# Performance work log

Hardware: AMD Instinct MI355X
Metric: run time of the kernel (lower is better)

## Reference

```python
import jax, jax.numpy as jnp
import numpy as np

SET_NUM, SET_SIZE, C, H, F, L_LAYERS, N_BLOCKS = 2048, 36, 192, 8, 384, 8, 4
N = SET_NUM * SET_SIZE


def _ln(x, g, b, eps=1e-5):
    m = x.mean(-1, keepdims=True)
    v = ((x - m) ** 2).mean(-1, keepdims=True)
    return (x - m) * jax.lax.rsqrt(v + eps) * g + b


def setup_inputs() -> dict:
    key = jax.random.key(0)
    ks = jax.random.split(key, 32)
    src = jax.random.normal(ks[0], (N, C), dtype=jnp.float32)
    pos_embed = jax.random.normal(ks[1], (2, N, C), dtype=jnp.float32)
    # each (shift, set) index tensor is a permutation of arange(N) -> every voxel appears exactly once
    perms = [jax.random.permutation(ks[2 + j], N).reshape(SET_NUM, SET_SIZE) for j in range(4)]
    set_voxel_inds = jnp.stack([jnp.stack(perms[0:2]), jnp.stack(perms[2:4])]).astype(jnp.int32)
    set_voxel_masks = jnp.zeros((2, 2, SET_NUM, SET_SIZE), dtype=bool)

    def p(k, shape, std=0.02):
        return (jax.random.normal(k, shape) * std).astype(jnp.float32)

    inp = dict(src=src, pos_embed=pos_embed, set_voxel_inds=set_voxel_inds,
               set_voxel_masks=set_voxel_masks,
               in_proj_w=p(ks[6], (L_LAYERS, 3 * C, C)), in_proj_b=p(ks[7], (L_LAYERS, 3 * C)),
               out_w=p(ks[8], (L_LAYERS, C, C)), out_b=p(ks[9], (L_LAYERS, C)),
               lin1_w=p(ks[10], (L_LAYERS, F, C)), lin1_b=p(ks[11], (L_LAYERS, F)),
               lin2_w=p(ks[12], (L_LAYERS, C, F)), lin2_b=p(ks[13], (L_LAYERS, C)),
               ln1_g=jnp.ones((L_LAYERS, C)), ln1_b=jnp.zeros((L_LAYERS, C)),
               ln2_g=jnp.ones((L_LAYERS, C)), ln2_b=jnp.zeros((L_LAYERS, C)),
               enc_g=jnp.ones((L_LAYERS, C)), enc_b=jnp.zeros((L_LAYERS, C)),
               blk_g=jnp.ones((N_BLOCKS, C)), blk_b=jnp.zeros((N_BLOCKS, C)))
    return inp


def reference(src, pos_embed, set_voxel_inds, set_voxel_masks,
              in_proj_w, in_proj_b, out_w, out_b, lin1_w, lin1_b, lin2_w, lin2_b,
              ln1_g, ln1_b, ln2_g, ln2_b, enc_g, enc_b, blk_g, blk_b):
    n_vox = src.shape[0]
    Dh = C // H
    scale = 1.0 / np.sqrt(Dh)

    def set_attn(x, pos, inds, mask, li):
        g = x[inds]                      # (S,K,C) gather voxels into sets
        qk_in = g + pos[inds]
        Wq, Wk, Wv = jnp.split(in_proj_w[li], 3, axis=0)
        bq, bk, bv = jnp.split(in_proj_b[li], 3)
        S, K = inds.shape
        q = (qk_in @ Wq.T + bq).reshape(S, K, H, Dh)
        k = (qk_in @ Wk.T + bk).reshape(S, K, H, Dh)
        v = (g @ Wv.T + bv).reshape(S, K, H, Dh)
        scores = jnp.einsum('skhd,slhd->shkl', q, k) * scale
        scores = jnp.where(mask[:, None, None, :], -1e9, scores)
        attn = jax.nn.softmax(scores, axis=-1)
        o = jnp.einsum('shkl,slhd->skhd', attn, v).reshape(S, K, C)
        o = o @ out_w[li].T + out_b[li]
        # torch.unique + flipped scatter == take the first occurrence of each voxel index
        flat = inds.reshape(-1)
        first = jnp.full((n_vox,), flat.size, dtype=flat.dtype).at[flat].min(
            jnp.arange(flat.size, dtype=flat.dtype))
        src2 = o.reshape(-1, C)[first]
        x = _ln(x + src2, ln1_g[li], ln1_b[li])
        ff = jax.nn.gelu(x @ lin1_w[li].T + lin1_b[li], approximate=False) @ lin2_w[li].T + lin2_b[li]
        x = _ln(x + ff, ln2_g[li], ln2_b[li])
        return x

    out = src
    for block_id in range(N_BLOCKS):
        residual = out
        shift = block_id % 2
        for i in range(2):
            li = block_id * 2 + i
            identity = out
            out = set_attn(out, pos_embed[i], set_voxel_inds[shift, i],
                           set_voxel_masks[shift, i], li)
            out = _ln(out + identity, enc_g[li], enc_b[li])
        out = _ln(out + residual, blk_g[block_id], blk_b[block_id])
    return out
```

## Files before the change

### kernel.cpp

```cpp
#include <hip/hip_runtime.h>
#include <hip/hip_bf16.h>
#include <hip/hip_fp16.h>

#define SETS 2048
#define SS   36
#define CDIM 192
#define HEADS 8
#define DH   24
#define FDIM 384
#define NVOX (SETS*SS)
#define NBLOCKS 4

typedef __hip_bfloat16 bf16;
typedef _Float16 f16;
typedef __attribute__((ext_vector_type(2))) _Float16 h2v;
typedef __attribute__((ext_vector_type(4))) short s4v;
typedef __attribute__((ext_vector_type(8))) short s8v;
typedef __attribute__((ext_vector_type(4))) float f4v;

__device__ __forceinline__ float to_f(float x) { return x; }
__device__ __forceinline__ float to_f(bf16 x)  { return __bfloat162float(x); }

__device__ __forceinline__ short f2bf(float x) {
  bf16 h = __float2bfloat16(x);
  return *reinterpret_cast<short*>(&h);
}
__device__ __forceinline__ unsigned pack2(float a, float b) {
  return ((unsigned)(unsigned short)f2bf(a)) | (((unsigned)(unsigned short)f2bf(b)) << 16);
}

__device__ __forceinline__ float dot2(unsigned a, unsigned b, float acc) {
#if __has_builtin(__builtin_amdgcn_fdot2)
  return __builtin_amdgcn_fdot2(__builtin_bit_cast(h2v, a), __builtin_bit_cast(h2v, b), acc, false);
#else
  h2v ha = __builtin_bit_cast(h2v, a), hb = __builtin_bit_cast(h2v, b);
  return acc + (float)ha[0] * (float)hb[0] + (float)ha[1] * (float)hb[1];
#endif
}
__device__ __forceinline__ unsigned pkh(float a, float b) {
#if __has_builtin(__builtin_amdgcn_cvt_pkrtz)
  return __builtin_bit_cast(unsigned, __builtin_amdgcn_cvt_pkrtz(a, b));
#else
  h2v h; h[0] = (f16)a; h[1] = (f16)b;
  return __builtin_bit_cast(unsigned, h);
#endif
}
__device__ __forceinline__ unsigned permw(unsigned a, unsigned b, unsigned sel) {
#if __has_builtin(__builtin_amdgcn_perm)
  return __builtin_amdgcn_perm(b, a, sel);
#else
  if (sel == 0x05040100u) return (a & 0xffffu) | (b << 16);
  return (a >> 16) | (b & 0xffff0000u);
#endif
}

__device__ __forceinline__ float allreduce64(float v) {
  #pragma unroll
  for (int off = 32; off > 0; off >>= 1) v += __shfl_xor(v, off);
  return v;
}

__device__ __forceinline__ void ln3(float v[3], const float* g, const float* b, int t) {
  float s = allreduce64(v[0] + v[1] + v[2]);
  float m = s * (1.0f / 192.0f);
  float d0 = v[0] - m, d1 = v[1] - m, d2 = v[2] - m;
  float q = allreduce64(d0 * d0 + d1 * d1 + d2 * d2);
  float rs = rsqrtf(q * (1.0f / 192.0f) + 1e-5f);
  v[0] = d0 * rs * g[t]       + b[t];
  v[1] = d1 * rs * g[t + 64]  + b[t + 64];
  v[2] = d2 * rs * g[t + 128] + b[t + 128];
}

__global__ __launch_bounds__(256) void wconv_k(const float* __restrict__ in,
                                               bf16* __restrict__ out, int n8) {
  int i = blockIdx.x * 256 + threadIdx.x;
  if (i < n8) {
    const float4* p = (const float4*)in + (size_t)i * 2;
    float4 a = p[0], b = p[1];
    s8v o;
    o[0] = f2bf(a.x); o[1] = f2bf(a.y); o[2] = f2bf(a.z); o[3] = f2bf(a.w);
    o[4] = f2bf(b.x); o[5] = f2bf(b.y); o[6] = f2bf(b.z); o[7] = f2bf(b.w);
    ((s8v*)out)[i] = o;
  }
}

__global__ __launch_bounds__(256) void init_k(const float* __restrict__ src,
    const float* __restrict__ pos0, float* __restrict__ a0,
    bf16* __restrict__ xb, bf16* __restrict__ xpb) {
  int i = blockIdx.x * 256 + threadIdx.x;
  float4 s = ((const float4*)src)[i];
  float4 p = ((const float4*)pos0)[i];
  ((float4*)a0)[i] = s;
  s4v ob, op;
  ob[0] = f2bf(s.x); ob[1] = f2bf(s.y); ob[2] = f2bf(s.z); ob[3] = f2bf(s.w);
  op[0] = f2bf(s.x + p.x); op[1] = f2bf(s.y + p.y);
  op[2] = f2bf(s.z + p.z); op[3] = f2bf(s.w + p.w);
  ((s4v*)xb)[i]  = ob;
  ((s4v*)xpb)[i] = op;
}

template<typename TO> __device__ __forceinline__ TO fcast(float v);
template<> __device__ __forceinline__ bf16 fcast<bf16>(float v) { return __float2bfloat16(v); }
template<> __device__ __forceinline__ f16  fcast<f16>(float v)  { return (f16)v; }

template<typename TO, int KT, int BM, int BN, int WM, int WN, bool GATHER, bool GELU_ACT>
__global__ __launch_bounds__(WM*WN*64) void bgemm_k(
    const bf16* __restrict__ A, const bf16* __restrict__ W,
    const float* __restrict__ bias, TO* __restrict__ Cmat,
    const int* __restrict__ idx, int ldc, int c_off)
{
  constexpr int NTHR = WM * WN * 64;
  constexpr int LD = 40;
  constexpr int MI = BM / (16 * WM);
  constexpr int NJ = BN / (16 * WN);
  constexpr int AC = BM * 4 / NTHR;
  constexpr int BC = BN * 4 / NTHR;
  constexpr int NT = KT / 32;
  static_assert(AC * NTHR == BM * 4 && BC * NTHR == BN * 4, "staging chunks");

  __shared__ short As[2][BM * LD];
  __shared__ short Bs[2][BN * LD];

  const int tid = threadIdx.x;
  const int n0 = blockIdx.x * BN;
  const int m0 = blockIdx.y * BM;
  const int wave = tid >> 6, lane = tid & 63;
  const int quad = lane >> 4, l16 = lane & 15;
  const int wm = (wave / WN) * (MI * 16);
  const int wn = (wave % WN) * (NJ * 16);

  const bf16* Aptr[AC]; int aoff[AC];
  #pragma unroll
  for (int c = 0; c < AC; c++) {
    int u = tid + c * NTHR;
    int row = u >> 2, c4 = u & 3;
    long arow = GATHER ? (long)idx[m0 + row] : (long)(m0 + row);
    Aptr[c] = A + arow * (long)KT + c4 * 8;
    aoff[c] = row * LD + c4 * 8;
  }
  const bf16* Bptr[BC]; int boff[BC];
  #pragma unroll
  for (int c = 0; c < BC; c++) {
    int u = tid + c * NTHR;
    int row = u >> 2, c4 = u & 3;
    Bptr[c] = W + (long)(n0 + row) * KT + c4 * 8;
    boff[c] = row * LD + c4 * 8;
  }

  uint4 ra[AC], rb[BC];
  #pragma unroll
  for (int c = 0; c < AC; c++) ra[c] = *(const uint4*)(Aptr[c]);
  #pragma unroll
  for (int c = 0; c < BC; c++) rb[c] = *(const uint4*)(Bptr[c]);
  #pragma unroll
  for (int c = 0; c < AC; c++) *(uint4*)&As[0][aoff[c]] = ra[c];
  #pragma unroll
  for (int c = 0; c < BC; c++) *(uint4*)&Bs[0][boff[c]] = rb[c];
  __syncthreads();

  f4v acc[MI][NJ];
  #pragma unroll
  for (int i = 0; i < MI; i++)
    #pragma unroll
    for (int j = 0; j < NJ; j++)
      #pragma unroll
      for (int r = 0; r < 4; r++) acc[i][j][r] = 0.f;

  #pragma unroll
  for (int t = 0; t < NT; t++) {
    const int cur = t & 1;
    if (t + 1 < NT) {
      #pragma unroll
      for (int c = 0; c < AC; c++) ra[c] = *(const uint4*)(Aptr[c] + (t + 1) * 32);
      #pragma unroll
      for (int c = 0; c < BC; c++) rb[c] = *(const uint4*)(Bptr[c] + (t + 1) * 32);
    }
    s8v af[MI], bfv[NJ];
    #pragma unroll
    for (int i = 0; i < MI; i++)
      af[i] = *(const s8v*)&As[cur][(wm + i * 16 + l16) * LD + quad * 8];
    #pragma unroll
    for (int j = 0; j < NJ; j++)
      bfv[j] = *(const s8v*)&Bs[cur][(wn + j * 16 + l16) * LD + quad * 8];
    #pragma unroll
    for (int i = 0; i < MI; i++)
      #pragma unroll
      for (int j = 0; j < NJ; j++)
        acc[i][j] = __builtin_amdgcn_mfma_f32_16x16x32_bf16(af[i], bfv[j], acc[i][j], 0, 0, 0);
    if (t + 1 < NT) {
      #pragma unroll
      for (int c = 0; c < AC; c++) *(uint4*)&As[cur ^ 1][aoff[c]] = ra[c];
      #pragma unroll
      for (int c = 0; c < BC; c++) *(uint4*)&Bs[cur ^ 1][boff[c]] = rb[c];
      __syncthreads();
    }
  }

  #pragma unroll
  for (int j = 0; j < NJ; j++) {
    int gn = n0 + wn + j * 16 + l16;
    float bj = bias[gn];
    #pragma unroll
    for (int i = 0; i < MI; i++) {
      #pragma unroll
      for (int r = 0; r < 4; r++) {
        int gm = m0 + wm + i * 16 + quad * 4 + r;
        float vv = acc[i][j][r] + bj;
        if (GELU_ACT) vv = 0.5f * vv * (1.0f + erff(vv * 0.70710678118654752f));
        Cmat[(long)gm * ldc + c_off + gn] = fcast<TO>(vv);
      }
    }
  }
}

#define KLD 392
__global__ __launch_bounds__(288) void attn_set_k(const f16* __restrict__ qkv,
                                                  bf16* __restrict__ o)
{
  __shared__ short kv[SS * KLD];
  const int s = blockIdx.x;
  const int tid = threadIdx.x;

  const int h = tid / SS;
  const int r = tid - h * SS;

  const uint4* qp = (const uint4*)(qkv + ((size_t)s * SS + r) * 576 + h * DH);
  uint4 uq0 = qp[0], uq1 = qp[1], uq2 = qp[2];

  const uint4* gp = (const uint4*)(qkv + (size_t)s * (SS * 576));
  uint4* ls = (uint4*)kv;
  #pragma unroll
  for (int i = 0; i < 6; i++) {
    int u = tid + i * 288;
    int row = u / 48;
    int c = u - row * 48;
    ls[row * 49 + c] = gp[row * 72 + 24 + c];
  }
  __syncthreads();

  unsigned qw[12] = { uq0.x, uq0.y, uq0.z, uq0.w,
                      uq1.x, uq1.y, uq1.z, uq1.w,
                      uq2.x, uq2.y, uq2.z, uq2.w };

  const float scale = 0.20412414523193154f;
  float sc[SS];
  #pragma unroll
  for (int l = 0; l < SS; l++) {
    const uint4* kp = (const uint4*)&kv[l * KLD + h * DH];
    uint4 u0 = kp[0], u1 = kp[1], u2 = kp[2];
    float a0 = 0.f, a1 = 0.f, a2 = 0.f;
    a0 = dot2(qw[0], u0.x, a0); a0 = dot2(qw[1], u0.y, a0);
    a0 = dot2(qw[2], u0.z, a0); a0 = dot2(qw[3], u0.w, a0);
    a1 = dot2(qw[4], u1.x, a1); a1 = dot2(qw[5], u1.y, a1);
    a1 = dot2(qw[6], u1.z, a1); a1 = dot2(qw[7], u1.w, a1);
    a2 = dot2(qw[8], u2.x, a2); a2 = dot2(qw[9], u2.y, a2);
    a2 = dot2(qw[10], u2.z, a2); a2 = dot2(qw[11], u2.w, a2);
    sc[l] = (a0 + a1 + a2) * scale;
  }

  float mx = -1e30f;
  #pragma unroll
  for (int l = 0; l < SS; l++) mx = fmaxf(mx, sc[l]);
  float sum = 0.f;
  #pragma unroll
  for (int l = 0; l < SS; l++) { float e = __expf(sc[l] - mx); sc[l] = e; sum += e; }
  float inv = 1.0f / sum;

  float ov[DH];
  #pragma unroll
  for (int d = 0; d < DH; d++) ov[d] = 0.f;
  #pragma unroll
  for (int lp = 0; lp < SS / 2; lp++) {
    const uint4* va = (const uint4*)&kv[(2 * lp) * KLD + 192 + h * DH];
    const uint4* vb = (const uint4*)&kv[(2 * lp + 1) * KLD + 192 + h * DH];
    unsigned pp = pkh(sc[2 * lp], sc[2 * lp + 1]);
    #pragma unroll
    for (int i = 0; i < 3; i++) {
      uint4 ua = va[i], ub = vb[i];
      unsigned wa[4] = { ua.x, ua.y, ua.z, ua.w };
      unsigned wb[4] = { ub.x, ub.y, ub.z, ub.w };
      #pragma unroll
      for (int j = 0; j < 4; j++) {
        unsigned lo = permw(wa[j], wb[j], 0x05040100u);
        unsigned hi = permw(wa[j], wb[j], 0x07060302u);
        ov[8*i + 2*j]     = dot2(pp, lo, ov[8*i + 2*j]);
        ov[8*i + 2*j + 1] = dot2(pp, hi, ov[8*i + 2*j + 1]);
      }
    }
  }

  uint4* op = (uint4*)(o + ((size_t)s * SS + r) * CDIM + h * DH);
  #pragma unroll
  for (int i = 0; i < 3; i++) {
    uint4 u;
    u.x = pack2(ov[8*i+0] * inv, ov[8*i+1] * inv);
    u.y = pack2(ov[8*i+2] * inv, ov[8*i+3] * inv);
    u.z = pack2(ov[8*i+4] * inv, ov[8*i+5] * inv);
    u.w = pack2(ov[8*i+6] * inv, ov[8*i+7] * inv);
    op[i] = u;
  }
}

__global__ __launch_bounds__(256) void scatter_ln1_k(
    const float* __restrict__ xin, const bf16* __restrict__ o2,
    const int* __restrict__ inds, const float* __restrict__ g,
    const float* __restrict__ b, float* __restrict__ x1,
    bf16* __restrict__ x1b)
{
  int p = blockIdx.x * 4 + (threadIdx.x >> 6);
  int t = threadIdx.x & 63;
  int vox = inds[p];
  long vb = (long)vox * 192, pb = (long)p * 192;
  float v[3];
  #pragma unroll
  for (int j = 0; j < 3; j++) { int c = t + 64 * j; v[j] = xin[vb + c] + to_f(o2[pb + c]); }
  ln3(v, g, b, t);
  #pragma unroll
  for (int j = 0; j < 3; j++) {
    int c = t + 64 * j;
    x1[vb + c]  = v[j];
    x1b[vb + c] = __float2bfloat16(v[j]);
  }
}

template<bool HAS_BLK, bool WRITE_OUT>
__global__ __launch_bounds__(256) void ln_chain_k(
    const float* __restrict__ x1, const bf16* __restrict__ ff,
    const float* __restrict__ identity, const float* __restrict__ resid,
    const float* __restrict__ g2, const float* __restrict__ b2,
    const float* __restrict__ ge, const float* __restrict__ be,
    const float* __restrict__ gb, const float* __restrict__ bb,
    float* __restrict__ outf, float* __restrict__ outd,
    const float* __restrict__ posn, bf16* __restrict__ xbo,
    bf16* __restrict__ xpo)
{
  int row = blockIdx.x * 4 + (threadIdx.x >> 6);
  int t = threadIdx.x & 63;
  long base = (long)row * 192;
  float v[3];
  #pragma unroll
  for (int j = 0; j < 3; j++) { int c = t + 64 * j; v[j] = x1[base + c] + to_f(ff[base + c]); }
  ln3(v, g2, b2, t);
  #pragma unroll
  for (int j = 0; j < 3; j++) { int c = t + 64 * j; v[j] += identity[base + c]; }
  ln3(v, ge, be, t);
  if (HAS_BLK) {
    #pragma unroll
    for (int j = 0; j < 3; j++) { int c = t + 64 * j; v[j] += resid[base + c]; }
    ln3(v, gb, bb, t);
  }
  #pragma unroll
  for (int j = 0; j < 3; j++) {
    int c = t + 64 * j;
    outf[base + c] = v[j];
    if (WRITE_OUT) outd[base + c] = v[j];
  }
  if (xbo) {
    #pragma unroll
    for (int j = 0; j < 3; j++) { int c = t + 64 * j; xbo[base + c] = __float2bfloat16(v[j]); }
  }
  if (xpo) {
    #pragma unroll
    for (int j = 0; j < 3; j++) {
      int c = t + 64 * j;
      xpo[base + c] = __float2bfloat16(v[j] + posn[base + c]);
    }
  }
}

extern "C" void kernel_launch(void* const* d_in, const int* in_sizes, int n_in,
                              void* d_out, int out_size, void* d_ws, size_t ws_size,
                              hipStream_t stream)
{
  const float* src       = (const float*)d_in[0];
  const float* pos_embed = (const float*)d_in[1];
  const int*   svi       = (const int*)d_in[2];
  const float* ipw  = (const float*)d_in[4];
  const float* ipb  = (const float*)d_in[5];
  const float* outw = (const float*)d_in[6];
  const float* outb = (const float*)d_in[7];
  const float* l1w  = (const float*)d_in[8];
  const float* l1b  = (const float*)d_in[9];
  const float* l2w  = (const float*)d_in[10];
  const float* l2b  = (const float*)d_in[11];
  const float* ln1g = (const float*)d_in[12];
  const float* ln1b = (const float*)d_in[13];
  const float* ln2g = (const float*)d_in[14];
  const float* ln2b = (const float*)d_in[15];
  const float* encg = (const float*)d_in[16];
  const float* encb = (const float*)d_in[17];
  const float* blkg = (const float*)d_in[18];
  const float* blkb = (const float*)d_in[19];

  char* w = (char*)d_ws;
  const size_t ACT  = (size_t)NVOX * CDIM * sizeof(float);
  const size_t QKVB = (size_t)NVOX * 576 * sizeof(f16);
  const size_t OB   = (size_t)NVOX * CDIM * sizeof(bf16);
  float* act[3] = { (float*)w, (float*)(w + ACT), (float*)(w + 2 * ACT) };
  f16*  qkv   = (f16*)(w + 3 * ACT);
  bf16* obuf  = (bf16*)(w + 3 * ACT + QKVB);
  bf16* o2buf = (bf16*)(w + 3 * ACT + QKVB + OB);
  bf16* xb    = o2buf;
  bf16* xpb   = (bf16*)(w + 3 * ACT + QKVB + 2 * OB);
  bf16* wbf   = (bf16*)(w + 3 * ACT + QKVB + 3 * OB);
  bf16* wip_b  = wbf;
  bf16* wout_b = wip_b  + (size_t)8 * 576 * 192;
  bf16* wl1_b  = wout_b + (size_t)8 * 192 * 192;
  bf16* wl2_b  = wl1_b  + (size_t)8 * 384 * 192;
  bf16* hbuf  = (bf16*)qkv;
  bf16* ffbuf = obuf;

  wconv_k<<<(8*576*192/8 + 255)/256, 256, 0, stream>>>(ipw,  wip_b,  8*576*192/8);
  wconv_k<<<(8*192*192/8 + 255)/256, 256, 0, stream>>>(outw, wout_b, 8*192*192/8);
  wconv_k<<<(8*384*192/8 + 255)/256, 256, 0, stream>>>(l1w,  wl1_b,  8*384*192/8);
  wconv_k<<<(8*192*384/8 + 255)/256, 256, 0, stream>>>(l2w,  wl2_b,  8*192*384/8);

  init_k<<<NVOX * CDIM / 4 / 256, 256, 0, stream>>>(src, pos_embed, act[0], xb, xpb);

  int r = 0, ia = 1, ib = 2;
  for (int blkid = 0; blkid < NBLOCKS; blkid++) {
    int shift = blkid & 1;
    float* xres = act[r];
    float* cur  = act[r];
    float* outs[2] = { act[ia], act[ib] };
    for (int i = 0; i < 2; i++) {
      int li = blkid * 2 + i;
      const int* inds = svi + (size_t)(shift * 2 + i) * SETS * SS;
      const float* Bip = ipb + (size_t)li * 576;

      bgemm_k<f16, 192, 128, 128, 2, 2, true, false>
          <<<dim3(3, NVOX / 128), 256, 0, stream>>>(
          xpb, wip_b + (size_t)li * 576 * 192, Bip, qkv, inds, 576, 0);
      bgemm_k<f16, 192, 128, 64, 4, 1, true, false>
          <<<dim3(3, NVOX / 128), 256, 0, stream>>>(
          xb, wip_b + (size_t)li * 576 * 192 + (size_t)384 * 192, Bip + 384, qkv,
          inds, 576, 384);

      attn_set_k<<<SETS, 288, 0, stream>>>(qkv, obuf);

      bgemm_k<bf16, 192, 128, 64, 4, 1, false, false>
          <<<dim3(3, NVOX / 128), 256, 0, stream>>>(
          obuf, wout_b + (size_t)li * 192 * 192, outb + (size_t)li * 192, o2buf,
          nullptr, 192, 0);

      float* x1 = outs[i];
      scatter_ln1_k<<<NVOX / 4, 256, 0, stream>>>(cur, o2buf, inds,
          ln1g + (size_t)li * 192, ln1b + (size_t)li * 192, x1, xpb );

      bgemm_k<bf16, 192, 128, 128, 2, 2, false, true>
          <<<dim3(3, NVOX / 128), 256, 0, stream>>>(
          xpb , wl1_b + (size_t)li * 384 * 192, l1b + (size_t)li * 384, hbuf,
          nullptr, 384, 0);
      bgemm_k<bf16, 384, 128, 64, 4, 1, false, false>
          <<<dim3(3, NVOX / 128), 256, 0, stream>>>(
          hbuf, wl2_b + (size_t)li * 192 * 384, l2b + (size_t)li * 192, ffbuf,
          nullptr, 192, 0);

      bool isFinal = (blkid == NBLOCKS - 1 && i == 1);
      const float* posn = pos_embed + (size_t)((li + 1) & 1) * NVOX * CDIM;
      if (i == 1) {
        if (isFinal)
          ln_chain_k<true, true><<<NVOX / 4, 256, 0, stream>>>(x1, ffbuf, cur, xres,
              ln2g + (size_t)li * 192, ln2b + (size_t)li * 192,
              encg + (size_t)li * 192, encb + (size_t)li * 192,
              blkg + (size_t)blkid * 192, blkb + (size_t)blkid * 192,
              x1, (float*)d_out, nullptr, nullptr, nullptr);
        else
          ln_chain_k<true, false><<<NVOX / 4, 256, 0, stream>>>(x1, ffbuf, cur, xres,
              ln2g + (size_t)li * 192, ln2b + (size_t)li * 192,
              encg + (size_t)li * 192, encb + (size_t)li * 192,
              blkg + (size_t)blkid * 192, blkb + (size_t)blkid * 192,
              x1, nullptr, posn, xb, xpb);
      } else {
        ln_chain_k<false, false><<<NVOX / 4, 256, 0, stream>>>(x1, ffbuf, cur, xres,
            ln2g + (size_t)li * 192, ln2b + (size_t)li * 192,
            encg + (size_t)li * 192, encb + (size_t)li * 192,
            nullptr, nullptr, x1, nullptr, posn, xb, xpb);
      }
      cur = x1;
    }
    int newr = ib, na = r, nb = ia;
    r = newr; ia = na; ib = nb;
  }
}
```

Baseline: 2.641 ms.

## Move set gather into attention kernel and keep activations in voxel order

The QKV GEMMs now run on voxel-ordered rows with no index gather. The attention kernel loads each set's member indices and gathers Q/K/V rows from the voxel-ordered buffer, then writes its output straight back to voxel positions. This removes the gather from the GEMM A-loads and the scatter from the LN1 kernel, which becomes a plain row-wise LN. The GEMM also remaps block IDs so that consecutive blocks are spread across 8 interleaved chunks, likely to match the XCD dispatch order. The cost is that the attention kernel's loads become scattered row reads.

```diff
diff --git a/kernel.cpp b/kernel.cpp
--- a/kernel.cpp
+++ b/kernel.cpp
@@ -103,11 +103,11 @@
 template<> __device__ __forceinline__ bf16 fcast<bf16>(float v) { return __float2bfloat16(v); }
 template<> __device__ __forceinline__ f16  fcast<f16>(float v)  { return (f16)v; }
 
-template<typename TO, int KT, int BM, int BN, int WM, int WN, bool GATHER, bool GELU_ACT>
+template<typename TO, int KT, int BM, int BN, int WM, int WN, bool GELU_ACT>
 __global__ __launch_bounds__(WM*WN*64) void bgemm_k(
     const bf16* __restrict__ A, const bf16* __restrict__ W,
     const float* __restrict__ bias, TO* __restrict__ Cmat,
-    const int* __restrict__ idx, int ldc, int c_off)
+    int ldc, int c_off)
 {
   constexpr int NTHR = WM * WN * 64;
   constexpr int LD = 40;
@@ -122,8 +122,12 @@
   __shared__ short Bs[2][BN * LD];
 
   const int tid = threadIdx.x;
-  const int n0 = blockIdx.x * BN;
-  const int m0 = blockIdx.y * BM;
+  const int gx = gridDim.x;
+  const int flat = blockIdx.y * gx + blockIdx.x;
+  const int chunk = (gx * gridDim.y) >> 3;
+  const int work = (flat & 7) * chunk + (flat >> 3);
+  const int n0 = (work % gx) * BN;
+  const int m0 = (work / gx) * BM;
   const int wave = tid >> 6, lane = tid & 63;
   const int quad = lane >> 4, l16 = lane & 15;
   const int wm = (wave / WN) * (MI * 16);
@@ -134,8 +138,7 @@
   for (int c = 0; c < AC; c++) {
     int u = tid + c * NTHR;
     int row = u >> 2, c4 = u & 3;
-    long arow = GATHER ? (long)idx[m0 + row] : (long)(m0 + row);
-    Aptr[c] = A + arow * (long)KT + c4 * 8;
+    Aptr[c] = A + (long)(m0 + row) * KT + c4 * 8;
     aoff[c] = row * LD + c4 * 8;
   }
   const bf16* Bptr[BC]; int boff[BC];
@@ -215,26 +218,32 @@
 
 #define KLD 392
 __global__ __launch_bounds__(288) void attn_set_k(const f16* __restrict__ qkv,
+                                                  const int* __restrict__ inds,
                                                   bf16* __restrict__ o)
 {
   __shared__ short kv[SS * KLD];
+  __shared__ int si[SS];
   const int s = blockIdx.x;
   const int tid = threadIdx.x;
 
+  if (tid < SS) si[tid] = inds[s * SS + tid];
+  __syncthreads();
+
   const int h = tid / SS;
   const int r = tid - h * SS;
-
-  const uint4* qp = (const uint4*)(qkv + ((size_t)s * SS + r) * 576 + h * DH);
+  const int vr = si[r];
+
+  const uint4* qp = (const uint4*)(qkv + (size_t)vr * 576 + h * DH);
   uint4 uq0 = qp[0], uq1 = qp[1], uq2 = qp[2];
 
-  const uint4* gp = (const uint4*)(qkv + (size_t)s * (SS * 576));
+  const uint4* gp = (const uint4*)qkv;
   uint4* ls = (uint4*)kv;
   #pragma unroll
   for (int i = 0; i < 6; i++) {
     int u = tid + i * 288;
     int row = u / 48;
     int c = u - row * 48;
-    ls[row * 49 + c] = gp[row * 72 + 24 + c];
+    ls[row * 49 + c] = gp[(size_t)si[row] * 72 + 24 + c];
   }
   __syncthreads();
 
@@ -289,7 +298,7 @@
     }
   }
 
-  uint4* op = (uint4*)(o + ((size_t)s * SS + r) * CDIM + h * DH);
+  uint4* op = (uint4*)(o + (size_t)vr * CDIM + h * DH);
   #pragma unroll
   for (int i = 0; i < 3; i++) {
     uint4 u;
@@ -301,25 +310,23 @@
   }
 }
 
-__global__ __launch_bounds__(256) void scatter_ln1_k(
+__global__ __launch_bounds__(256) void ln1_k(
     const float* __restrict__ xin, const bf16* __restrict__ o2,
-    const int* __restrict__ inds, const float* __restrict__ g,
-    const float* __restrict__ b, float* __restrict__ x1,
-    bf16* __restrict__ x1b)
+    const float* __restrict__ g, const float* __restrict__ b,
+    float* __restrict__ x1, bf16* __restrict__ x1b)
 {
   int p = blockIdx.x * 4 + (threadIdx.x >> 6);
   int t = threadIdx.x & 63;
-  int vox = inds[p];
-  long vb = (long)vox * 192, pb = (long)p * 192;
+  long base = (long)p * 192;
   float v[3];
   #pragma unroll
-  for (int j = 0; j < 3; j++) { int c = t + 64 * j; v[j] = xin[vb + c] + to_f(o2[pb + c]); }
+  for (int j = 0; j < 3; j++) { int c = t + 64 * j; v[j] = xin[base + c] + to_f(o2[base + c]); }
   ln3(v, g, b, t);
   #pragma unroll
   for (int j = 0; j < 3; j++) {
     int c = t + 64 * j;
-    x1[vb + c]  = v[j];
-    x1b[vb + c] = __float2bfloat16(v[j]);
+    x1[base + c]  = v[j];
+    x1b[base + c] = __float2bfloat16(v[j]);
   }
 }
 
@@ -428,33 +435,33 @@
       const int* inds = svi + (size_t)(shift * 2 + i) * SETS * SS;
       const float* Bip = ipb + (size_t)li * 576;
 
-      bgemm_k<f16, 192, 128, 128, 2, 2, true, false>
+      bgemm_k<f16, 192, 128, 128, 2, 2, false>
           <<<dim3(3, NVOX / 128), 256, 0, stream>>>(
-          xpb, wip_b + (size_t)li * 576 * 192, Bip, qkv, inds, 576, 0);
-      bgemm_k<f16, 192, 128, 64, 4, 1, true, false>
+          xpb, wip_b + (size_t)li * 576 * 192, Bip, qkv, 576, 0);
+      bgemm_k<f16, 192, 128, 64, 4, 1, false>
           <<<dim3(3, NVOX / 128), 256, 0, stream>>>(
           xb, wip_b + (size_t)li * 576 * 192 + (size_t)384 * 192, Bip + 384, qkv,
-          inds, 576, 384);
-
-      attn_set_k<<<SETS, 288, 0, stream>>>(qkv, obuf);
-
-      bgemm_k<bf16, 192, 128, 64, 4, 1, false, false>
+          576, 384);
+
+      attn_set_k<<<SETS, 288, 0, stream>>>(qkv, inds, obuf);
+
+      bgemm_k<bf16, 192, 128, 64, 4, 1, false>
           <<<dim3(3, NVOX / 128), 256, 0, stream>>>(
           obuf, wout_b + (size_t)li * 192 * 192, outb + (size_t)li * 192, o2buf,
-          nullptr, 192, 0);
+          192, 0);
 
       float* x1 = outs[i];
-      scatter_ln1_k<<<NVOX / 4, 256, 0, stream>>>(cur, o2buf, inds,
+      ln1_k<<<NVOX / 4, 256, 0, stream>>>(cur, o2buf,
           ln1g + (size_t)li * 192, ln1b + (size_t)li * 192, x1, xpb );
 
-      bgemm_k<bf16, 192, 128, 128, 2, 2, false, true>
+      bgemm_k<bf16, 192, 128, 128, 2, 2, true>
           <<<dim3(3, NVOX / 128), 256, 0, stream>>>(
           xpb , wl1_b + (size_t)li * 384 * 192, l1b + (size_t)li * 384, hbuf,
-          nullptr, 384, 0);
-      bgemm_k<bf16, 384, 128, 64, 4, 1, false, false>
+          384, 0);
+      bgemm_k<bf16, 384, 128, 64, 4, 1, false>
           <<<dim3(3, NVOX / 128), 256, 0, stream>>>(
           hbuf, wl2_b + (size_t)li * 192 * 384, l2b + (size_t)li * 192, ffbuf,
-          nullptr, 192, 0);
+          192, 0);
 
       bool isFinal = (blkid == NBLOCKS - 1 && i == 1);
       const float* posn = pos_embed + (size_t)((li + 1) & 1) * NVOX * CDIM;
```

New measurement: 2.446 ms. 1.08x faster.
